# Performance work log

Measured on AMD Instinct MI355X. Metric: run time of the kernel, lower is better.

Reference implementation:

```python
import jax, jax.numpy as jnp
import numpy as np

N, FIN, FOUT = 4096, 256, 256


def setup_inputs() -> dict:
    key = jax.random.key(0)
    ks = jax.random.split(key, 6)
    x = jax.random.normal(ks[0], (N, FIN), jnp.float32)
    adj = jax.random.randint(ks[1], (N, N), 0, 2, jnp.int32)  # dense 0/1 adjacency
    W = jax.random.normal(ks[2], (FOUT, FIN), jnp.float32) / np.sqrt(FIN)
    b = jax.random.normal(ks[3], (FOUT,), jnp.float32) * 0.01
    att_w = jax.random.normal(ks[4], (2 * FOUT,), jnp.float32) / np.sqrt(2.0 * FOUT)  # Linear(2F,1).weight squeezed
    att_b = jax.random.normal(ks[5], (), jnp.float32) * 0.01
    return {"x": x, "adj": adj, "W": W, "b": b, "att_w": att_w, "att_b": att_b}


def reference(x, adj, W, b, att_w, att_b):
    n = x.shape[0]
    fo = W.shape[0]
    h = x @ W.T + b  # [N, Fout]
    # score(i,j) = att([h_i ; h_j]) = h_i.w1 + h_j.w2 + att_b  -> no [N,N,2F] concat
    s = (h @ att_w[:fo])[:, None] + (h @ att_w[fo:])[None, :] + att_b  # [N, N]
    edge = adj == 1
    # GLOBAL softmax over all edges (faithful to F.softmax(stacked_scores, dim=0))
    gmax = jnp.max(jnp.where(edge, s, -jnp.inf))
    e = jnp.exp(s - gmax)
    denom = jnp.sum(jnp.where(edge, e, 0.0))
    p = (e / denom).reshape(-1)  # softmaxed score per pair (valid at edges)
    # original indexes attention_scores[j] by NODE id j into the row-major edge list:
    # recover the score of the j-th global edge (j = 0..N-1) via cumsum rank + scatter
    flat = edge.reshape(-1)
    rank = jnp.cumsum(flat.astype(jnp.int32)) - 1  # rank of each edge in row-major order
    idx = jnp.where(flat, rank, n)  # non-edges and ranks >= n get dropped
    w_node = jnp.zeros((n,), h.dtype).at[idx].set(p, mode="drop")  # [N]
    # output[i] = sum_{j: adj[i,j]==1} w_node[j] * h[j]
    out = jax.nn.relu(edge.astype(h.dtype) @ (w_node[:, None] * h))
    return out
```

## Files before the change

kernel.cpp:

```cpp
#include <hip/hip_runtime.h>
#include <cstdint>
#include <cstddef>

#define NN 4096
#define FDIM 256

typedef __attribute__((ext_vector_type(4))) float fx4;
typedef __attribute__((ext_vector_type(2))) float fx2;
typedef __attribute__((ext_vector_type(8))) short s8v;

__device__ inline uint16_t f2bf(float f) {
    union { float f; uint32_t u; } v; v.f = f;
    uint32_t u = v.u;
    uint32_t r = (u + 0x7FFFu + ((u >> 16) & 1u)) >> 16;
    return (uint16_t)r;
}

__global__ __launch_bounds__(512) void k_h(const float* __restrict__ x,
        const float* __restrict__ W, const float* __restrict__ bias,
        const float* __restrict__ att_w, float* __restrict__ h,
        float* __restrict__ a1p, float* __restrict__ a2p) {
    __shared__ __align__(16) float xs[2][64 * 68];
    __shared__ __align__(16) float wt[2][64 * 68];
    const int bi = blockIdx.x, bf = blockIdx.y;
    const int t = threadIdx.x;
    const int t256 = t & 255;
    const int kh = t >> 8;
    const int tx = t256 & 15, ty = t256 >> 4;
    float acc[4][4] = {};
    float rx[8], rw[8];
    #pragma unroll
    for (int u = 0; u < 8; ++u) {
        const int e = t + 512 * u, r = e >> 6, c = e & 63;
        rx[u] = x[(size_t)(bi * 64 + r) * 256 + c];
        rw[u] = W[(size_t)(bf * 64 + r) * 256 + c];
    }
    for (int p = 0; p < 4; ++p) {
        float* xb = xs[p & 1];
        float* wb = wt[p & 1];
        #pragma unroll
        for (int u = 0; u < 8; ++u) {
            const int e = t + 512 * u, r = e >> 6, c = e & 63;
            const int sw = 8 * ((c & 7) ^ ((c >> 3) & 7));
            xb[c * 68 + (r ^ sw)] = rx[u];
            wb[c * 68 + (r ^ sw)] = rw[u];
        }
        __syncthreads();
        if (p < 3) {
            const int k0 = (p + 1) * 64;
            #pragma unroll
            for (int u = 0; u < 8; ++u) {
                const int e = t + 512 * u, r = e >> 6, c = e & 63;
                rx[u] = x[(size_t)(bi * 64 + r) * 256 + k0 + c];
                rw[u] = W[(size_t)(bf * 64 + r) * 256 + k0 + c];
            }
        }
        #pragma unroll 8
        for (int k = 0; k < 32; ++k) {
            const int kk = kh * 32 + k;
            const int sw = 8 * ((kk & 7) ^ ((kk >> 3) & 7));
            const fx4 av = *(const fx4*)(xb + kk * 68 + ((ty * 4) ^ sw));
            const fx4 bv = *(const fx4*)(wb + kk * 68 + ((tx * 4) ^ sw));
            #pragma unroll
            for (int u = 0; u < 4; ++u)
                #pragma unroll
                for (int v = 0; v < 4; ++v)
                    acc[u][v] += av[u] * bv[v];
        }
    }
    __syncthreads();
    float* cbuf = xs[0];
    if (kh == 1) {
        #pragma unroll
        for (int u = 0; u < 4; ++u)
            *(fx4*)(cbuf + t256 * 16 + u * 4) = *(const fx4*)(&acc[u][0]);
    }
    __syncthreads();
    if (kh == 0) {
        #pragma unroll
        for (int u = 0; u < 4; ++u) {
            const fx4 o = *(const fx4*)(cbuf + t256 * 16 + u * 4);
            #pragma unroll
            for (int v = 0; v < 4; ++v) acc[u][v] += o[v];
        }
        const fx4 bv = *(const fx4*)(bias + bf * 64 + tx * 4);
        const fx4 w1v = *(const fx4*)(att_w + bf * 64 + tx * 4);
        const fx4 w2v = *(const fx4*)(att_w + 256 + bf * 64 + tx * 4);
        #pragma unroll
        for (int u = 0; u < 4; ++u) {
            const int i = bi * 64 + ty * 4 + u;
            fx4 r;
            float s1 = 0.f, s2 = 0.f;
            #pragma unroll
            for (int v = 0; v < 4; ++v) {
                r[v] = acc[u][v] + bv[v];
                s1 += r[v] * w1v[v];
                s2 += r[v] * w2v[v];
            }
            *(fx4*)(h + (size_t)i * 256 + bf * 64 + tx * 4) = r;
            #pragma unroll
            for (int d = 8; d > 0; d >>= 1) {
                s1 += __shfl_down(s1, d, 16);
                s2 += __shfl_down(s2, d, 16);
            }
            if (tx == 0) {
                a1p[bf * NN + i] = s1;
                a2p[bf * NN + i] = s2;
            }
        }
    }
}

__global__ __launch_bounds__(1024) void k_prep(const float* __restrict__ a1p,
        const float* __restrict__ a2p, const int* __restrict__ adj,
        float* __restrict__ E1, float* __restrict__ E2,
        float* __restrict__ wraw, float* __restrict__ Sg) {
    __shared__ float E1s[NN];
    __shared__ float E2s[NN];
    __shared__ float red1[16], red2[16];
    __shared__ int wtot[16];
    __shared__ int base_s;
    const int t = threadIdx.x, lane = t & 63, wv = t >> 6;
    fx4 v1 = {0.f, 0.f, 0.f, 0.f}, v2 = {0.f, 0.f, 0.f, 0.f};
    #pragma unroll
    for (int bf = 0; bf < 4; ++bf) {
        v1 += *(const fx4*)(a1p + bf * NN + t * 4);
        v2 += *(const fx4*)(a2p + bf * NN + t * 4);
    }
    float m1 = fmaxf(fmaxf(v1[0], v1[1]), fmaxf(v1[2], v1[3]));
    float m2 = fmaxf(fmaxf(v2[0], v2[1]), fmaxf(v2[2], v2[3]));
    #pragma unroll
    for (int d = 32; d > 0; d >>= 1) {
        m1 = fmaxf(m1, __shfl_down(m1, d));
        m2 = fmaxf(m2, __shfl_down(m2, d));
    }
    if (lane == 0) { red1[wv] = m1; red2[wv] = m2; }
    __syncthreads();
    if (t == 0) {
        float mm1 = -1e30f, mm2 = -1e30f;
        for (int k = 0; k < 16; ++k) {
            mm1 = fmaxf(mm1, red1[k]);
            mm2 = fmaxf(mm2, red2[k]);
        }
        red1[0] = mm1; red2[0] = mm2;
        *Sg = 0.f;
        base_s = 0;
    }
    __syncthreads();
    const float M1 = red1[0], M2 = red2[0];
    fx4 e1v, e2v, z4 = {0.f, 0.f, 0.f, 0.f};
    #pragma unroll
    for (int j = 0; j < 4; ++j) {
        e1v[j] = expf(v1[j] - M1);
        e2v[j] = expf(v2[j] - M2);
    }
    *(fx4*)(E1s + t * 4) = e1v;
    *(fx4*)(E2s + t * 4) = e2v;
    *(fx4*)(E1 + t * 4) = e1v;
    *(fx4*)(E2 + t * 4) = e2v;
    *(fx4*)(wraw + t * 4) = z4;
    __syncthreads();
    for (int row = 0; row < NN; ++row) {
        const int base = base_s;
        if (base >= NN) break;
        const int4 a = ((const int4*)(adj + (size_t)row * NN))[t];
        const int vj[4] = {a.x, a.y, a.z, a.w};
        int cnt = 0;
        #pragma unroll
        for (int j = 0; j < 4; ++j) cnt += (vj[j] == 1);
        int inc = cnt;
        #pragma unroll
        for (int d = 1; d < 64; d <<= 1) {
            const int y = __shfl_up(inc, d);
            if (lane >= d) inc += y;
        }
        if (lane == 63) wtot[wv] = inc;
        __syncthreads();
        int wbase = 0, total = 0;
        #pragma unroll
        for (int w = 0; w < 16; ++w) {
            const int xw = wtot[w];
            total += xw;
            wbase += (w < wv) ? xw : 0;
        }
        if (t == 0) base_s = base + total;
        int r = base + wbase + inc - cnt;
        if (cnt && r < NN) {
            const float e1 = E1s[row];
            #pragma unroll
            for (int j = 0; j < 4; ++j) {
                if (vj[j] == 1) {
                    if (r < NN) wraw[r] = e1 * E2s[t * 4 + j];
                    ++r;
                }
            }
        }
        __syncthreads();
    }
}

__global__ __launch_bounds__(256) void k_g(const float* __restrict__ h,
        const float* __restrict__ wraw, uint16_t* __restrict__ gt) {
    __shared__ float tile[64 * 33];
    const int bj = blockIdx.x, bf = blockIdx.y;
    const int j0 = bj * 64, f0 = bf * 32;
    const int t = threadIdx.x;
    #pragma unroll
    for (int p = 0; p < 8; ++p) {
        const int e = t + 256 * p;
        const int jl = e >> 5, fl = e & 31;
        tile[jl * 33 + fl] = h[(size_t)(j0 + jl) * 256 + f0 + fl] * wraw[j0 + jl];
    }
    __syncthreads();
    {
        const int fl = t >> 3, cb = t & 7;
        const int phys_cb = cb ^ (fl & 7);
        s8v v;
        #pragma unroll
        for (int lo = 0; lo < 8; ++lo)
            v[lo] = (short)f2bf(tile[(cb * 8 + lo) * 33 + fl]);
        *(s8v*)(gt + (size_t)(f0 + fl) * NN + j0 + phys_cb * 8) = v;
    }
}

__global__ __launch_bounds__(256) void k_fused(const int* __restrict__ adj,
        const uint16_t* __restrict__ gt, const float* __restrict__ E1,
        const float* __restrict__ E2, uint16_t* __restrict__ part,
        float* __restrict__ Sg, int krange) {
    __shared__ __align__(16) uint16_t As[64 * 72];
    __shared__ __align__(16) uint16_t Gs[256 * 64];
    __shared__ __align__(16) uint16_t GsS[16 * 72];
    const int ib = blockIdx.x, ks = blockIdx.y;
    const int t = threadIdx.x;
    const int wv = t >> 6, lane = t & 63;
    const int q = lane >> 4, m16 = lane & 15;
    const int i0 = ib * 64, k0 = ks * krange;
    const int ksteps = krange >> 6;
    fx4 acc[4][4];
    #pragma unroll
    for (int a = 0; a < 4; ++a)
        #pragma unroll
        for (int b = 0; b < 4; ++b) acc[a][b] = (fx4){0.f, 0.f, 0.f, 0.f};
    fx4 accS[4];
    #pragma unroll
    for (int a = 0; a < 4; ++a) accS[a] = (fx4){0.f, 0.f, 0.f, 0.f};
    for (int e = t; e < 15 * 72; e += 256) GsS[72 + e] = 0;

    const int fr = lane >> 3, cb = lane & 7;
    const int ar = t >> 4, ac4 = (t & 15) * 4;
    int4 ra[4];
    #pragma unroll
    for (int p = 0; p < 4; ++p)
        ra[p] = *(const int4*)(adj + (size_t)(i0 + p * 16 + ar) * NN + k0 + ac4);

    for (int step = 0; step < ksteps; ++step) {
        const int kk = k0 + step * 64;
        #pragma unroll
        for (int p = 0; p < 4; ++p) {
            uint2 w;
            w.x = (uint32_t)(ra[p].x | (ra[p].y << 16)) * 0x3F80u;
            w.y = (uint32_t)(ra[p].z | (ra[p].w << 16)) * 0x3F80u;
            *(uint2*)(&As[(p * 16 + ar) * 72 + ac4]) = w;
        }
        #pragma unroll
        for (int p = 0; p < 8; ++p) {
            const int f0 = wv * 64 + p * 8;
            const uint16_t* gp = gt + (size_t)(f0 + fr) * NN + kk + cb * 8;
            __builtin_amdgcn_global_load_lds(
                (const __attribute__((address_space(1))) uint32_t*)gp,
                (__attribute__((address_space(3))) uint32_t*)(Gs + f0 * 64),
                16, 0, 0);
        }
        if (t < 8) {
            const float* e2p = E2 + kk + t * 8;
            uint32_t* dst = (uint32_t*)(&GsS[t * 8]);
            #pragma unroll
            for (int j = 0; j < 4; ++j)
                dst[j] = (uint32_t)f2bf(e2p[2 * j]) |
                         ((uint32_t)f2bf(e2p[2 * j + 1]) << 16);
        }
        __syncthreads();
        if (step + 1 < ksteps) {
            #pragma unroll
            for (int p = 0; p < 4; ++p)
                ra[p] = *(const int4*)(adj + (size_t)(i0 + p * 16 + ar) * NN +
                                       kk + 64 + ac4);
        }
        s8v afr[4][2];
        #pragma unroll
        for (int it = 0; it < 4; ++it)
            #pragma unroll
            for (int kh = 0; kh < 2; ++kh)
                afr[it][kh] = *(const s8v*)(As + (it * 16 + m16) * 72 + kh * 32 + q * 8);
        #pragma unroll
        for (int ft = 0; ft < 4; ++ft) {
            #pragma unroll
            for (int kh = 0; kh < 2; ++kh) {
                const int row = wv * 64 + ft * 16 + m16;
                const int pcb = ((kh << 2) | q) ^ (m16 & 7);
                const s8v bfr = *(const s8v*)(Gs + row * 64 + pcb * 8);
                #pragma unroll
                for (int it = 0; it < 4; ++it)
                    acc[it][ft] = __builtin_amdgcn_mfma_f32_16x16x32_bf16(
                        afr[it][kh], bfr, acc[it][ft], 0, 0, 0);
            }
        }
        if (wv == 3) {
            #pragma unroll
            for (int kh = 0; kh < 2; ++kh) {
                const s8v bfrS = *(const s8v*)(GsS + m16 * 72 + kh * 32 + q * 8);
                #pragma unroll
                for (int it = 0; it < 4; ++it)
                    accS[it] = __builtin_amdgcn_mfma_f32_16x16x32_bf16(
                        afr[it][kh], bfrS, accS[it], 0, 0, 0);
            }
        }
        __syncthreads();
    }
    if (wv == 3) {
        float s_local = 0.f;
        #pragma unroll
        for (int it = 0; it < 4; ++it)
            #pragma unroll
            for (int r = 0; r < 4; ++r)
                s_local += accS[it][r] * E1[i0 + it * 16 + q * 4 + r];
        #pragma unroll
        for (int d = 32; d > 0; d >>= 1) s_local += __shfl_down(s_local, d);
        if (lane == 0) atomicAdd(Sg, s_local);
    }
    uint16_t* dst = part + (size_t)ks * NN * FDIM;
    #pragma unroll
    for (int it = 0; it < 4; ++it) {
        #pragma unroll
        for (int ft = 0; ft < 4; ++ft) {
            const int f = wv * 64 + ft * 16 + m16;
            #pragma unroll
            for (int r = 0; r < 4; ++r) {
                const int i = i0 + it * 16 + q * 4 + r;
                dst[(size_t)i * FDIM + f] = f2bf(acc[it][ft][r]);
            }
        }
    }
}

__global__ __launch_bounds__(256) void k_out(const uint16_t* __restrict__ part,
        const float* __restrict__ Sg, float* __restrict__ out, int nsplit) {
    const size_t idx = ((size_t)blockIdx.x * 256 + threadIdx.x) * 8;
    const float inv = 1.0f / (*Sg);
    float s[8] = {};
    for (int k = 0; k < nsplit; ++k) {
        const s8v v = *(const s8v*)(part + (size_t)k * NN * FDIM + idx);
        #pragma unroll
        for (int j = 0; j < 8; ++j) {
            union { uint32_t u; float f; } cv;
            cv.u = ((uint32_t)(uint16_t)v[j]) << 16;
            s[j] += cv.f;
        }
    }
    fx4 r0, r1;
    #pragma unroll
    for (int j = 0; j < 4; ++j) {
        r0[j] = fmaxf(s[j], 0.f) * inv;
        r1[j] = fmaxf(s[4 + j], 0.f) * inv;
    }
    *(fx4*)(out + idx) = r0;
    *(fx4*)(out + idx + 4) = r1;
}

extern "C" void kernel_launch(void* const* d_in, const int* in_sizes, int n_in,
                              void* d_out, int out_size, void* d_ws, size_t ws_size,
                              hipStream_t stream) {
    const float* x     = (const float*)d_in[0];
    const int*   adj   = (const int*)d_in[1];
    const float* W     = (const float*)d_in[2];
    const float* bias  = (const float*)d_in[3];
    const float* att_w = (const float*)d_in[4];
    float* out = (float*)d_out;
    char* ws = (char*)d_ws;
    float*    h    = (float*)(ws + 0);
    uint16_t* gt   = (uint16_t*)(ws + (size_t)4194304);
    float*    a1p  = (float*)(ws + 6291456);
    float*    a2p  = (float*)(ws + 6356992);
    float*    E1   = (float*)(ws + 6422528);
    float*    E2   = (float*)(ws + 6438912);
    float*    wraw = (float*)(ws + 6455296);
    float*    Sg   = (float*)(ws + 6471680);
    uint16_t* part = (uint16_t*)(ws + 6471936);

    const size_t avail = (ws_size > 6471936) ? (ws_size - 6471936) : 0;
    int splitk = 1;
    while (splitk < 8 &&
           (size_t)(splitk * 2) * NN * FDIM * sizeof(uint16_t) <= avail)
        splitk <<= 1;
    const int krange = NN / splitk;

    k_h    <<<dim3(64, 4), 512, 0, stream>>>(x, W, bias, att_w, h, a1p, a2p);
    k_prep <<<dim3(1), 1024, 0, stream>>>(a1p, a2p, adj, E1, E2, wraw, Sg);
    k_g    <<<dim3(64, 8), 256, 0, stream>>>(h, wraw, gt);
    k_fused<<<dim3(64, splitk), 256, 0, stream>>>(adj, gt, E1, E2, part, Sg, krange);
    k_out  <<<dim3(512), 256, 0, stream>>>(part, Sg, out, splitk);
}
```

Baseline: 146.0 us.

## Fuse all GAT stages into one persistent kernel with grid barriers

Replaces the five separate kernels with a single 256-block persistent kernel that uses atomic-counter grid barriers between phases. The h GEMM now writes the transposed bf16 tile directly, so the separate transpose and scale pass over h is dropped. The aggregation phase uses global_load_lds prefetching and 512-thread blocks with an in-block reduction across wave halves. This removes launch overhead and intermediate traffic, but relies on all blocks being co-resident and serialises the single-block rank scan inside the fused kernel.

After: 287.1 us. 1.97x slower.

```diff
diff --git a/kernel.cpp b/kernel.cpp
--- a/kernel.cpp
+++ b/kernel.cpp
@@ -4,367 +4,413 @@
 
 #define NN 4096
 #define FDIM 256
+#define NBLK 256
 
 typedef __attribute__((ext_vector_type(4))) float fx4;
-typedef __attribute__((ext_vector_type(2))) float fx2;
 typedef __attribute__((ext_vector_type(8))) short s8v;
+
+__device__ int g_cnt;
+__device__ int g_flag;
 
 __device__ inline uint16_t f2bf(float f) {
     union { float f; uint32_t u; } v; v.f = f;
-    uint32_t u = v.u;
-    uint32_t r = (u + 0x7FFFu + ((u >> 16) & 1u)) >> 16;
-    return (uint16_t)r;
+    const uint32_t u = v.u;
+    return (uint16_t)((u + 0x7FFFu + ((u >> 16) & 1u)) >> 16);
 }
 
-__global__ __launch_bounds__(512) void k_h(const float* __restrict__ x,
+struct ShA { float xs[2][64 * 68]; float wt[2][64 * 68]; };
+struct ShP { float E1s[NN]; float E2s[NN]; float red1[8]; float red2[8];
+             int wtot[8]; int base_s; };
+struct ShF { uint16_t As[2][64 * 72]; uint16_t Gs[2][256 * 64]; };
+union ShMem { ShA a; ShP p; ShF f; float cex[4][64 * 68]; };
+
+__device__ __forceinline__ void gbar(int target) {
+    __syncthreads();
+    if (threadIdx.x == 0) {
+        __threadfence();
+        const int prev = __hip_atomic_fetch_add(&g_cnt, 1, __ATOMIC_ACQ_REL,
+                                                __HIP_MEMORY_SCOPE_AGENT);
+        if (prev == target * NBLK - 1) {
+            __hip_atomic_store(&g_flag, target, __ATOMIC_RELEASE,
+                               __HIP_MEMORY_SCOPE_AGENT);
+        } else {
+            while (__hip_atomic_load(&g_flag, __ATOMIC_ACQUIRE,
+                                     __HIP_MEMORY_SCOPE_AGENT) < target)
+                __builtin_amdgcn_s_sleep(2);
+        }
+        __threadfence();
+    }
+    __syncthreads();
+}
+
+__global__ __launch_bounds__(512, 2) void gat_all(
+        const float* __restrict__ x, const int* __restrict__ adj,
         const float* __restrict__ W, const float* __restrict__ bias,
-        const float* __restrict__ att_w, float* __restrict__ h,
-        float* __restrict__ a1p, float* __restrict__ a2p) {
-    __shared__ __align__(16) float xs[2][64 * 68];
-    __shared__ __align__(16) float wt[2][64 * 68];
-    const int bi = blockIdx.x, bf = blockIdx.y;
+        const float* __restrict__ att_w, uint16_t* __restrict__ gt,
+        float* __restrict__ a1p, float* __restrict__ a2p,
+        float* __restrict__ E1, float* __restrict__ E2,
+        float* __restrict__ wraw, float* __restrict__ Sg,
+        uint16_t* __restrict__ part, float* __restrict__ out) {
+    __shared__ __align__(16) ShMem sh;
+    __shared__ int sh_base;
     const int t = threadIdx.x;
-    const int t256 = t & 255;
-    const int kh = t >> 8;
-    const int tx = t256 & 15, ty = t256 >> 4;
-    float acc[4][4] = {};
-    float rx[8], rw[8];
-    #pragma unroll
-    for (int u = 0; u < 8; ++u) {
-        const int e = t + 512 * u, r = e >> 6, c = e & 63;
-        rx[u] = x[(size_t)(bi * 64 + r) * 256 + c];
-        rw[u] = W[(size_t)(bf * 64 + r) * 256 + c];
-    }
-    for (int p = 0; p < 4; ++p) {
-        float* xb = xs[p & 1];
-        float* wb = wt[p & 1];
+    const int b = blockIdx.x;
+    if (t == 0)
+        sh_base = __hip_atomic_load(&g_flag, __ATOMIC_RELAXED, __HIP_MEMORY_SCOPE_AGENT);
+    __syncthreads();
+    const int ep0 = sh_base;
+
+    {
+        const int bi = b & 63, bf = b >> 6;
+        const int t256 = t & 255;
+        const int kh = t >> 8;
+        const int tx = t256 & 15, ty = t256 >> 4;
+        float acc[4][4] = {};
+        float rx[8], rw[8];
         #pragma unroll
         for (int u = 0; u < 8; ++u) {
             const int e = t + 512 * u, r = e >> 6, c = e & 63;
-            const int sw = 8 * ((c & 7) ^ ((c >> 3) & 7));
-            xb[c * 68 + (r ^ sw)] = rx[u];
-            wb[c * 68 + (r ^ sw)] = rw[u];
-        }
-        __syncthreads();
-        if (p < 3) {
-            const int k0 = (p + 1) * 64;
+            rx[u] = x[(size_t)(bi * 64 + r) * 256 + c];
+            rw[u] = W[(size_t)(bf * 64 + r) * 256 + c];
+        }
+        for (int p = 0; p < 4; ++p) {
+            float* xb = sh.a.xs[p & 1];
+            float* wb = sh.a.wt[p & 1];
             #pragma unroll
             for (int u = 0; u < 8; ++u) {
                 const int e = t + 512 * u, r = e >> 6, c = e & 63;
-                rx[u] = x[(size_t)(bi * 64 + r) * 256 + k0 + c];
-                rw[u] = W[(size_t)(bf * 64 + r) * 256 + k0 + c];
-            }
-        }
-        #pragma unroll 8
-        for (int k = 0; k < 32; ++k) {
-            const int kk = kh * 32 + k;
-            const int sw = 8 * ((kk & 7) ^ ((kk >> 3) & 7));
-            const fx4 av = *(const fx4*)(xb + kk * 68 + ((ty * 4) ^ sw));
-            const fx4 bv = *(const fx4*)(wb + kk * 68 + ((tx * 4) ^ sw));
+                const int sw = 8 * ((c & 7) ^ ((c >> 3) & 7));
+                xb[c * 68 + (r ^ sw)] = rx[u];
+                wb[c * 68 + (r ^ sw)] = rw[u];
+            }
+            __syncthreads();
+            if (p < 3) {
+                const int kc = (p + 1) * 64;
+                #pragma unroll
+                for (int u = 0; u < 8; ++u) {
+                    const int e = t + 512 * u, r = e >> 6, c = e & 63;
+                    rx[u] = x[(size_t)(bi * 64 + r) * 256 + kc + c];
+                    rw[u] = W[(size_t)(bf * 64 + r) * 256 + kc + c];
+                }
+            }
+            #pragma unroll 8
+            for (int k = 0; k < 32; ++k) {
+                const int kk = kh * 32 + k;
+                const int sw = 8 * ((kk & 7) ^ ((kk >> 3) & 7));
+                const fx4 av = *(const fx4*)(xb + kk * 68 + ((ty * 4) ^ sw));
+                const fx4 bv = *(const fx4*)(wb + kk * 68 + ((tx * 4) ^ sw));
+                #pragma unroll
+                for (int u = 0; u < 4; ++u)
+                    #pragma unroll
+                    for (int v = 0; v < 4; ++v)
+                        acc[u][v] += av[u] * bv[v];
+            }
+        }
+        __syncthreads();
+        float* cbuf = sh.a.xs[0];
+        if (kh == 1) {
             #pragma unroll
             for (int u = 0; u < 4; ++u)
+                *(fx4*)(cbuf + t256 * 16 + u * 4) = *(const fx4*)(&acc[u][0]);
+        }
+        __syncthreads();
+        if (kh == 0) {
+            float* tileT = sh.a.wt[0];
+            #pragma unroll
+            for (int u = 0; u < 4; ++u) {
+                const fx4 o = *(const fx4*)(cbuf + t256 * 16 + u * 4);
+                #pragma unroll
+                for (int v = 0; v < 4; ++v) acc[u][v] += o[v];
+            }
+            const fx4 bv = *(const fx4*)(bias + bf * 64 + tx * 4);
+            const fx4 w1v = *(const fx4*)(att_w + bf * 64 + tx * 4);
+            const fx4 w2v = *(const fx4*)(att_w + 256 + bf * 64 + tx * 4);
+            #pragma unroll
+            for (int u = 0; u < 4; ++u) {
+                const int i = bi * 64 + ty * 4 + u;
+                fx4 r;
+                float s1 = 0.f, s2 = 0.f;
+                #pragma unroll
+                for (int v = 0; v < 4; ++v) {
+                    r[v] = acc[u][v] + bv[v];
+                    s1 += r[v] * w1v[v];
+                    s2 += r[v] * w2v[v];
+                }
                 #pragma unroll
                 for (int v = 0; v < 4; ++v)
-                    acc[u][v] += av[u] * bv[v];
-        }
-    }
-    __syncthreads();
-    float* cbuf = xs[0];
-    if (kh == 1) {
-        #pragma unroll
-        for (int u = 0; u < 4; ++u)
-            *(fx4*)(cbuf + t256 * 16 + u * 4) = *(const fx4*)(&acc[u][0]);
-    }
-    __syncthreads();
-    if (kh == 0) {
-        #pragma unroll
-        for (int u = 0; u < 4; ++u) {
-            const fx4 o = *(const fx4*)(cbuf + t256 * 16 + u * 4);
-            #pragma unroll
-            for (int v = 0; v < 4; ++v) acc[u][v] += o[v];
-        }
-        const fx4 bv = *(const fx4*)(bias + bf * 64 + tx * 4);
-        const fx4 w1v = *(const fx4*)(att_w + bf * 64 + tx * 4);
-        const fx4 w2v = *(const fx4*)(att_w + 256 + bf * 64 + tx * 4);
-        #pragma unroll
-        for (int u = 0; u < 4; ++u) {
-            const int i = bi * 64 + ty * 4 + u;
-            fx4 r;
-            float s1 = 0.f, s2 = 0.f;
-            #pragma unroll
-            for (int v = 0; v < 4; ++v) {
-                r[v] = acc[u][v] + bv[v];
-                s1 += r[v] * w1v[v];
-                s2 += r[v] * w2v[v];
-            }
-            *(fx4*)(h + (size_t)i * 256 + bf * 64 + tx * 4) = r;
-            #pragma unroll
-            for (int d = 8; d > 0; d >>= 1) {
-                s1 += __shfl_down(s1, d, 16);
-                s2 += __shfl_down(s2, d, 16);
-            }
-            if (tx == 0) {
-                a1p[bf * NN + i] = s1;
-                a2p[bf * NN + i] = s2;
-            }
-        }
-    }
-}
-
-__global__ __launch_bounds__(1024) void k_prep(const float* __restrict__ a1p,
-        const float* __restrict__ a2p, const int* __restrict__ adj,
-        float* __restrict__ E1, float* __restrict__ E2,
-        float* __restrict__ wraw, float* __restrict__ Sg) {
-    __shared__ float E1s[NN];
-    __shared__ float E2s[NN];
-    __shared__ float red1[16], red2[16];
-    __shared__ int wtot[16];
-    __shared__ int base_s;
-    const int t = threadIdx.x, lane = t & 63, wv = t >> 6;
-    fx4 v1 = {0.f, 0.f, 0.f, 0.f}, v2 = {0.f, 0.f, 0.f, 0.f};
+                    tileT[(tx * 4 + v) * 68 + ty * 4 + u] = r[v];
+                #pragma unroll
+                for (int d = 8; d > 0; d >>= 1) {
+                    s1 += __shfl_down(s1, d, 16);
+                    s2 += __shfl_down(s2, d, 16);
+                }
+                if (tx == 0) {
+                    a1p[bf * NN + i] = s1;
+                    a2p[bf * NN + i] = s2;
+                }
+            }
+        }
+        __syncthreads();
+        {
+            const float* tileT = sh.a.wt[0];
+            const int fl = t >> 3, cb = t & 7;
+            const int pcb = cb ^ (fl & 7);
+            s8v v;
+            #pragma unroll
+            for (int lo = 0; lo < 8; ++lo)
+                v[lo] = (short)f2bf(tileT[fl * 68 + cb * 8 + lo]);
+            *(s8v*)(gt + (size_t)(bf * 64 + fl) * NN + bi * 64 + pcb * 8) = v;
+        }
+    }
+
+    gbar(ep0 + 1);
+
+    const int ib = b & 63, ks = b >> 6;
+    const int i0 = ib * 64, k0f = ks * 1024;
+    const int wv = t >> 6, lane = t & 63;
+    const int ar = t >> 4, ac4 = (t & 15) * 4;
+    const int fr = lane >> 3, cbd = lane & 7;
+    int4 ra[2];
     #pragma unroll
-    for (int bf = 0; bf < 4; ++bf) {
-        v1 += *(const fx4*)(a1p + bf * NN + t * 4);
-        v2 += *(const fx4*)(a2p + bf * NN + t * 4);
-    }
-    float m1 = fmaxf(fmaxf(v1[0], v1[1]), fmaxf(v1[2], v1[3]));
-    float m2 = fmaxf(fmaxf(v2[0], v2[1]), fmaxf(v2[2], v2[3]));
+    for (int p = 0; p < 2; ++p)
+        ra[p] = *(const int4*)(adj + (size_t)(i0 + p * 32 + ar) * NN + k0f + ac4);
+
+    if (b == 0) {
+        const int wvi = t >> 6;
+        fx4 v1a = {0.f,0.f,0.f,0.f}, v1b = {0.f,0.f,0.f,0.f};
+        fx4 v2a = {0.f,0.f,0.f,0.f}, v2b = {0.f,0.f,0.f,0.f};
+        #pragma unroll
+        for (int bf = 0; bf < 4; ++bf) {
+            v1a += *(const fx4*)(a1p + bf * NN + t * 8);
+            v1b += *(const fx4*)(a1p + bf * NN + t * 8 + 4);
+            v2a += *(const fx4*)(a2p + bf * NN + t * 8);
+            v2b += *(const fx4*)(a2p + bf * NN + t * 8 + 4);
+        }
+        float m1 = fmaxf(fmaxf(fmaxf(v1a[0], v1a[1]), fmaxf(v1a[2], v1a[3])),
+                         fmaxf(fmaxf(v1b[0], v1b[1]), fmaxf(v1b[2], v1b[3])));
+        float m2 = fmaxf(fmaxf(fmaxf(v2a[0], v2a[1]), fmaxf(v2a[2], v2a[3])),
+                         fmaxf(fmaxf(v2b[0], v2b[1]), fmaxf(v2b[2], v2b[3])));
+        #pragma unroll
+        for (int d = 32; d > 0; d >>= 1) {
+            m1 = fmaxf(m1, __shfl_down(m1, d));
+            m2 = fmaxf(m2, __shfl_down(m2, d));
+        }
+        if (lane == 0) { sh.p.red1[wvi] = m1; sh.p.red2[wvi] = m2; }
+        __syncthreads();
+        if (t == 0) {
+            float mm1 = -1e30f, mm2 = -1e30f;
+            for (int k = 0; k < 8; ++k) {
+                mm1 = fmaxf(mm1, sh.p.red1[k]);
+                mm2 = fmaxf(mm2, sh.p.red2[k]);
+            }
+            sh.p.red1[0] = mm1; sh.p.red2[0] = mm2;
+            *Sg = 0.f;
+            sh.p.base_s = 0;
+        }
+        __syncthreads();
+        const float M1 = sh.p.red1[0], M2 = sh.p.red2[0];
+        fx4 e1a, e1b, e2a, e2b;
+        #pragma unroll
+        for (int j = 0; j < 4; ++j) {
+            e1a[j] = expf(v1a[j] - M1); e1b[j] = expf(v1b[j] - M1);
+            e2a[j] = expf(v2a[j] - M2); e2b[j] = expf(v2b[j] - M2);
+        }
+        *(fx4*)(sh.p.E1s + t * 8) = e1a; *(fx4*)(sh.p.E1s + t * 8 + 4) = e1b;
+        *(fx4*)(sh.p.E2s + t * 8) = e2a; *(fx4*)(sh.p.E2s + t * 8 + 4) = e2b;
+        *(fx4*)(E1 + t * 8) = e1a;       *(fx4*)(E1 + t * 8 + 4) = e1b;
+        *(fx4*)(E2 + t * 8) = e2a;       *(fx4*)(E2 + t * 8 + 4) = e2b;
+        const fx4 z4 = {0.f, 0.f, 0.f, 0.f};
+        *(fx4*)(wraw + t * 8) = z4;      *(fx4*)(wraw + t * 8 + 4) = z4;
+        __syncthreads();
+        for (int row = 0; row < NN; ++row) {
+            const int base = sh.p.base_s;
+            if (base >= NN) break;
+            const int4 a0 = ((const int4*)(adj + (size_t)row * NN))[t * 2];
+            const int4 a1v = ((const int4*)(adj + (size_t)row * NN))[t * 2 + 1];
+            const int vj[8] = {a0.x, a0.y, a0.z, a0.w, a1v.x, a1v.y, a1v.z, a1v.w};
+            int cnt = 0;
+            #pragma unroll
+            for (int j = 0; j < 8; ++j) cnt += (vj[j] == 1);
+            int inc = cnt;
+            #pragma unroll
+            for (int d = 1; d < 64; d <<= 1) {
+                const int y = __shfl_up(inc, d);
+                if (lane >= d) inc += y;
+            }
+            if (lane == 63) sh.p.wtot[wvi] = inc;
+            __syncthreads();
+            int wbase = 0, total = 0;
+            #pragma unroll
+            for (int w = 0; w < 8; ++w) {
+                const int xw = sh.p.wtot[w];
+                total += xw;
+                wbase += (w < wvi) ? xw : 0;
+            }
+            if (t == 0) sh.p.base_s = base + total;
+            int r = base + wbase + inc - cnt;
+            if (cnt && r < NN) {
+                const float e1 = sh.p.E1s[row];
+                #pragma unroll
+                for (int j = 0; j < 8; ++j) {
+                    if (vj[j] == 1) {
+                        if (r < NN) wraw[r] = e1 * sh.p.E2s[t * 8 + j];
+                        ++r;
+                    }
+                }
+            }
+            __syncthreads();
+        }
+    }
+
     #pragma unroll
-    for (int d = 32; d > 0; d >>= 1) {
-        m1 = fmaxf(m1, __shfl_down(m1, d));
-        m2 = fmaxf(m2, __shfl_down(m2, d));
-    }
-    if (lane == 0) { red1[wv] = m1; red2[wv] = m2; }
-    __syncthreads();
-    if (t == 0) {
-        float mm1 = -1e30f, mm2 = -1e30f;
-        for (int k = 0; k < 16; ++k) {
-            mm1 = fmaxf(mm1, red1[k]);
-            mm2 = fmaxf(mm2, red2[k]);
-        }
-        red1[0] = mm1; red2[0] = mm2;
-        *Sg = 0.f;
-        base_s = 0;
-    }
-    __syncthreads();
-    const float M1 = red1[0], M2 = red2[0];
-    fx4 e1v, e2v, z4 = {0.f, 0.f, 0.f, 0.f};
-    #pragma unroll
-    for (int j = 0; j < 4; ++j) {
-        e1v[j] = expf(v1[j] - M1);
-        e2v[j] = expf(v2[j] - M2);
-    }
-    *(fx4*)(E1s + t * 4) = e1v;
-    *(fx4*)(E2s + t * 4) = e2v;
-    *(fx4*)(E1 + t * 4) = e1v;
-    *(fx4*)(E2 + t * 4) = e2v;
-    *(fx4*)(wraw + t * 4) = z4;
-    __syncthreads();
-    for (int row = 0; row < NN; ++row) {
-        const int base = base_s;
-        if (base >= NN) break;
-        const int4 a = ((const int4*)(adj + (size_t)row * NN))[t];
-        const int vj[4] = {a.x, a.y, a.z, a.w};
-        int cnt = 0;
-        #pragma unroll
-        for (int j = 0; j < 4; ++j) cnt += (vj[j] == 1);
-        int inc = cnt;
-        #pragma unroll
-        for (int d = 1; d < 64; d <<= 1) {
-            const int y = __shfl_up(inc, d);
-            if (lane >= d) inc += y;
-        }
-        if (lane == 63) wtot[wv] = inc;
-        __syncthreads();
-        int wbase = 0, total = 0;
-        #pragma unroll
-        for (int w = 0; w < 16; ++w) {
-            const int xw = wtot[w];
-            total += xw;
-            wbase += (w < wv) ? xw : 0;
-        }
-        if (t == 0) base_s = base + total;
-        int r = base + wbase + inc - cnt;
-        if (cnt && r < NN) {
-            const float e1 = E1s[row];
-            #pragma unroll
-            for (int j = 0; j < 4; ++j) {
-                if (vj[j] == 1) {
-                    if (r < NN) wraw[r] = e1 * E2s[t * 4 + j];
-                    ++r;
-                }
-            }
-        }
-        __syncthreads();
-    }
-}
-
-__global__ __launch_bounds__(256) void k_g(const float* __restrict__ h,
-        const float* __restrict__ wraw, uint16_t* __restrict__ gt) {
-    __shared__ float tile[64 * 33];
-    const int bj = blockIdx.x, bf = blockIdx.y;
-    const int j0 = bj * 64, f0 = bf * 32;
-    const int t = threadIdx.x;
-    #pragma unroll
-    for (int p = 0; p < 8; ++p) {
-        const int e = t + 256 * p;
-        const int jl = e >> 5, fl = e & 31;
-        tile[jl * 33 + fl] = h[(size_t)(j0 + jl) * 256 + f0 + fl] * wraw[j0 + jl];
-    }
-    __syncthreads();
+    for (int p = 0; p < 4; ++p) {
+        const uint16_t* gp = gt + (size_t)(wv * 32 + p * 8 + fr) * NN + k0f + cbd * 8;
+        __builtin_amdgcn_global_load_lds(
+            (const __attribute__((address_space(1))) uint32_t*)gp,
+            (__attribute__((address_space(3))) uint32_t*)(&sh.f.Gs[0][(wv * 32 + p * 8) * 64]),
+            16, 0, 0);
+    }
+
+    gbar(ep0 + 2);
+
     {
-        const int fl = t >> 3, cb = t & 7;
-        const int phys_cb = cb ^ (fl & 7);
-        s8v v;
-        #pragma unroll
-        for (int lo = 0; lo < 8; ++lo)
-            v[lo] = (short)f2bf(tile[(cb * 8 + lo) * 33 + fl]);
-        *(s8v*)(gt + (size_t)(f0 + fl) * NN + j0 + phys_cb * 8) = v;
-    }
-}
-
-__global__ __launch_bounds__(256) void k_fused(const int* __restrict__ adj,
-        const uint16_t* __restrict__ gt, const float* __restrict__ E1,
-        const float* __restrict__ E2, uint16_t* __restrict__ part,
-        float* __restrict__ Sg, int krange) {
-    __shared__ __align__(16) uint16_t As[64 * 72];
-    __shared__ __align__(16) uint16_t Gs[256 * 64];
-    __shared__ __align__(16) uint16_t GsS[16 * 72];
-    const int ib = blockIdx.x, ks = blockIdx.y;
-    const int t = threadIdx.x;
-    const int wv = t >> 6, lane = t & 63;
-    const int q = lane >> 4, m16 = lane & 15;
-    const int i0 = ib * 64, k0 = ks * krange;
-    const int ksteps = krange >> 6;
-    fx4 acc[4][4];
-    #pragma unroll
-    for (int a = 0; a < 4; ++a)
-        #pragma unroll
-        for (int b = 0; b < 4; ++b) acc[a][b] = (fx4){0.f, 0.f, 0.f, 0.f};
-    fx4 accS[4];
-    #pragma unroll
-    for (int a = 0; a < 4; ++a) accS[a] = (fx4){0.f, 0.f, 0.f, 0.f};
-    for (int e = t; e < 15 * 72; e += 256) GsS[72 + e] = 0;
-
-    const int fr = lane >> 3, cb = lane & 7;
-    const int ar = t >> 4, ac4 = (t & 15) * 4;
-    int4 ra[4];
-    #pragma unroll
-    for (int p = 0; p < 4; ++p)
-        ra[p] = *(const int4*)(adj + (size_t)(i0 + p * 16 + ar) * NN + k0 + ac4);
-
-    for (int step = 0; step < ksteps; ++step) {
-        const int kk = k0 + step * 64;
-        #pragma unroll
-        for (int p = 0; p < 4; ++p) {
-            uint2 w;
-            w.x = (uint32_t)(ra[p].x | (ra[p].y << 16)) * 0x3F80u;
-            w.y = (uint32_t)(ra[p].z | (ra[p].w << 16)) * 0x3F80u;
-            *(uint2*)(&As[(p * 16 + ar) * 72 + ac4]) = w;
-        }
-        #pragma unroll
-        for (int p = 0; p < 8; ++p) {
-            const int f0 = wv * 64 + p * 8;
-            const uint16_t* gp = gt + (size_t)(f0 + fr) * NN + kk + cb * 8;
-            __builtin_amdgcn_global_load_lds(
-                (const __attribute__((address_space(1))) uint32_t*)gp,
-                (__attribute__((address_space(3))) uint32_t*)(Gs + f0 * 64),
-                16, 0, 0);
-        }
-        if (t < 8) {
-            const float* e2p = E2 + kk + t * 8;
-            uint32_t* dst = (uint32_t*)(&GsS[t * 8]);
-            #pragma unroll
-            for (int j = 0; j < 4; ++j)
-                dst[j] = (uint32_t)f2bf(e2p[2 * j]) |
-                         ((uint32_t)f2bf(e2p[2 * j + 1]) << 16);
-        }
-        __syncthreads();
-        if (step + 1 < ksteps) {
-            #pragma unroll
-            for (int p = 0; p < 4; ++p)
-                ra[p] = *(const int4*)(adj + (size_t)(i0 + p * 16 + ar) * NN +
-                                       kk + 64 + ac4);
-        }
-        s8v afr[4][2];
-        #pragma unroll
-        for (int it = 0; it < 4; ++it)
-            #pragma unroll
-            for (int kh = 0; kh < 2; ++kh)
-                afr[it][kh] = *(const s8v*)(As + (it * 16 + m16) * 72 + kh * 32 + q * 8);
-        #pragma unroll
-        for (int ft = 0; ft < 4; ++ft) {
-            #pragma unroll
-            for (int kh = 0; kh < 2; ++kh) {
-                const int row = wv * 64 + ft * 16 + m16;
-                const int pcb = ((kh << 2) | q) ^ (m16 & 7);
-                const s8v bfr = *(const s8v*)(Gs + row * 64 + pcb * 8);
+        const int q = lane >> 4, m16 = lane & 15;
+        const int khw = wv >> 2, fquad = wv & 3;
+        fx4 acc[4][4];
+        #pragma unroll
+        for (int a2 = 0; a2 < 4; ++a2)
+            #pragma unroll
+            for (int b2 = 0; b2 < 4; ++b2) acc[a2][b2] = (fx4){0.f, 0.f, 0.f, 0.f};
+        float sS = 0.f;
+        const float e1r0 = E1[i0 + ar];
+        const float e1r1 = E1[i0 + 32 + ar];
+        fx4 rw4 = *(const fx4*)(wraw + k0f + ac4);
+        fx4 re2 = *(const fx4*)(E2 + k0f + ac4);
+        {
+            const uint16_t wb0 = f2bf(rw4[0]), wb1 = f2bf(rw4[1]);
+            const uint16_t wb2 = f2bf(rw4[2]), wb3 = f2bf(rw4[3]);
+            #pragma unroll
+            for (int p = 0; p < 2; ++p) {
+                uint2 wo;
+                wo.x = (ra[p].x == 1 ? (uint32_t)wb0 : 0u) |
+                       ((ra[p].y == 1 ? (uint32_t)wb1 : 0u) << 16);
+                wo.y = (ra[p].z == 1 ? (uint32_t)wb2 : 0u) |
+                       ((ra[p].w == 1 ? (uint32_t)wb3 : 0u) << 16);
+                *(uint2*)(&sh.f.As[0][(p * 32 + ar) * 72 + ac4]) = wo;
+            }
+            sS += e1r0 * ((ra[0].x == 1 ? re2[0] : 0.f) + (ra[0].y == 1 ? re2[1] : 0.f) +
+                          (ra[0].z == 1 ? re2[2] : 0.f) + (ra[0].w == 1 ? re2[3] : 0.f));
+            sS += e1r1 * ((ra[1].x == 1 ? re2[0] : 0.f) + (ra[1].y == 1 ? re2[1] : 0.f) +
+                          (ra[1].z == 1 ? re2[2] : 0.f) + (ra[1].w == 1 ? re2[3] : 0.f));
+        }
+        __syncthreads();
+        const int pcb = ((khw << 2) | q) ^ (m16 & 7);
+        for (int stp = 0; stp < 16; ++stp) {
+            const int cur = stp & 1, nxt = cur ^ 1;
+            const int kk = k0f + stp * 64;
+            if (stp < 15) {
+                #pragma unroll
+                for (int p = 0; p < 4; ++p) {
+                    const uint16_t* gp =
+                        gt + (size_t)(wv * 32 + p * 8 + fr) * NN + kk + 64 + cbd * 8;
+                    __builtin_amdgcn_global_load_lds(
+                        (const __attribute__((address_space(1))) uint32_t*)gp,
+                        (__attribute__((address_space(3))) uint32_t*)(&sh.f.Gs[nxt][(wv * 32 + p * 8) * 64]),
+                        16, 0, 0);
+                }
+                #pragma unroll
+                for (int p = 0; p < 2; ++p)
+                    ra[p] = *(const int4*)(adj + (size_t)(i0 + p * 32 + ar) * NN +
+                                           kk + 64 + ac4);
+                rw4 = *(const fx4*)(wraw + kk + 64 + ac4);
+                re2 = *(const fx4*)(E2 + kk + 64 + ac4);
+            }
+            s8v afr[4];
+            #pragma unroll
+            for (int it = 0; it < 4; ++it)
+                afr[it] = *(const s8v*)(&sh.f.As[cur][(it * 16 + m16) * 72 + khw * 32 + q * 8]);
+            #pragma unroll
+            for (int ft = 0; ft < 4; ++ft) {
+                const int row = fquad * 64 + ft * 16 + m16;
+                const s8v bfr = *(const s8v*)(&sh.f.Gs[cur][row * 64 + pcb * 8]);
                 #pragma unroll
                 for (int it = 0; it < 4; ++it)
                     acc[it][ft] = __builtin_amdgcn_mfma_f32_16x16x32_bf16(
-                        afr[it][kh], bfr, acc[it][ft], 0, 0, 0);
-            }
-        }
-        if (wv == 3) {
-            #pragma unroll
-            for (int kh = 0; kh < 2; ++kh) {
-                const s8v bfrS = *(const s8v*)(GsS + m16 * 72 + kh * 32 + q * 8);
-                #pragma unroll
-                for (int it = 0; it < 4; ++it)
-                    accS[it] = __builtin_amdgcn_mfma_f32_16x16x32_bf16(
-                        afr[it][kh], bfrS, accS[it], 0, 0, 0);
-            }
-        }
-        __syncthreads();
-    }
-    if (wv == 3) {
-        float s_local = 0.f;
-        #pragma unroll
-        for (int it = 0; it < 4; ++it)
-            #pragma unroll
-            for (int r = 0; r < 4; ++r)
-                s_local += accS[it][r] * E1[i0 + it * 16 + q * 4 + r];
-        #pragma unroll
-        for (int d = 32; d > 0; d >>= 1) s_local += __shfl_down(s_local, d);
-        if (lane == 0) atomicAdd(Sg, s_local);
-    }
-    uint16_t* dst = part + (size_t)ks * NN * FDIM;
-    #pragma unroll
-    for (int it = 0; it < 4; ++it) {
-        #pragma unroll
-        for (int ft = 0; ft < 4; ++ft) {
-            const int f = wv * 64 + ft * 16 + m16;
-            #pragma unroll
-            for (int r = 0; r < 4; ++r) {
-                const int i = i0 + it * 16 + q * 4 + r;
-                dst[(size_t)i * FDIM + f] = f2bf(acc[it][ft][r]);
-            }
-        }
-    }
-}
-
-__global__ __launch_bounds__(256) void k_out(const uint16_t* __restrict__ part,
-        const float* __restrict__ Sg, float* __restrict__ out, int nsplit) {
-    const size_t idx = ((size_t)blockIdx.x * 256 + threadIdx.x) * 8;
-    const float inv = 1.0f / (*Sg);
-    float s[8] = {};
-    for (int k = 0; k < nsplit; ++k) {
-        const s8v v = *(const s8v*)(part + (size_t)k * NN * FDIM + idx);
-        #pragma unroll
-        for (int j = 0; j < 8; ++j) {
-            union { uint32_t u; float f; } cv;
-            cv.u = ((uint32_t)(uint16_t)v[j]) << 16;
-            s[j] += cv.f;
-        }
-    }
-    fx4 r0, r1;
-    #pragma unroll
-    for (int j = 0; j < 4; ++j) {
-        r0[j] = fmaxf(s[j], 0.f) * inv;
-        r1[j] = fmaxf(s[4 + j], 0.f) * inv;
-    }
-    *(fx4*)(out + idx) = r0;
-    *(fx4*)(out + idx + 4) = r1;
+                        afr[it], bfr, acc[it][ft], 0, 0, 0);
+            }
+            if (stp < 15) {
+                const uint16_t wb0 = f2bf(rw4[0]), wb1 = f2bf(rw4[1]);
+                const uint16_t wb2 = f2bf(rw4[2]), wb3 = f2bf(rw4[3]);
+                #pragma unroll
+                for (int p = 0; p < 2; ++p) {
+                    uint2 wo;
+                    wo.x = (ra[p].x == 1 ? (uint32_t)wb0 : 0u) |
+                           ((ra[p].y == 1 ? (uint32_t)wb1 : 0u) << 16);
+                    wo.y = (ra[p].z == 1 ? (uint32_t)wb2 : 0u) |
+                           ((ra[p].w == 1 ? (uint32_t)wb3 : 0u) << 16);
+                    *(uint2*)(&sh.f.As[nxt][(p * 32 + ar) * 72 + ac4]) = wo;
+                }
+                sS += e1r0 * ((ra[0].x == 1 ? re2[0] : 0.f) + (ra[0].y == 1 ? re2[1] : 0.f) +
+                              (ra[0].z == 1 ? re2[2] : 0.f) + (ra[0].w == 1 ? re2[3] : 0.f));
+                sS += e1r1 * ((ra[1].x == 1 ? re2[0] : 0.f) + (ra[1].y == 1 ? re2[1] : 0.f) +
+                              (ra[1].z == 1 ? re2[2] : 0.f) + (ra[1].w == 1 ? re2[3] : 0.f));
+            }
+            __syncthreads();
+        }
+        #pragma unroll
+        for (int d = 32; d > 0; d >>= 1) sS += __shfl_down(sS, d);
+        if (lane == 0) atomicAdd(Sg, sS);
+        if (wv >= 4) {
+            float* cx = &sh.cex[fquad][0] + lane * 68;
+            #pragma unroll
+            for (int it = 0; it < 4; ++it)
+                #pragma unroll
+                for (int ft = 0; ft < 4; ++ft)
+                    *(fx4*)(cx + it * 16 + ft * 4) = acc[it][ft];
+        }
+        __syncthreads();
+        if (wv < 4) {
+            const float* cx = &sh.cex[fquad][0] + lane * 68;
+            uint16_t* dst = part + (size_t)ks * NN * FDIM;
+            #pragma unroll
+            for (int it = 0; it < 4; ++it)
+                #pragma unroll
+                for (int ft = 0; ft < 4; ++ft) {
+                    const fx4 o = *(const fx4*)(cx + it * 16 + ft * 4);
+                    const int f = fquad * 64 + ft * 16 + m16;
+                    #pragma unroll
+                    for (int r = 0; r < 4; ++r)
+                        dst[(size_t)(i0 + it * 16 + q * 4 + r) * FDIM + f] =
+                            f2bf(acc[it][ft][r] + o[r]);
+                }
+        }
+    }
+
+    gbar(ep0 + 3);
+
+    {
+        const size_t idx = ((size_t)b * 512 + t) * 8;
+        const float inv = 1.0f / (*Sg);
+        float s[8] = {};
+        #pragma unroll
+        for (int k = 0; k < 4; ++k) {
+            const s8v v = *(const s8v*)(part + (size_t)k * NN * FDIM + idx);
+            #pragma unroll
+            for (int j = 0; j < 8; ++j) {
+                union { uint32_t u; float f; } cv;
+                cv.u = ((uint32_t)(uint16_t)v[j]) << 16;
+                s[j] += cv.f;
+            }
+        }
+        fx4 r0, r1;
+        #pragma unroll
+        for (int j = 0; j < 4; ++j) {
+            r0[j] = fmaxf(s[j], 0.f) * inv;
+            r1[j] = fmaxf(s[4 + j], 0.f) * inv;
+        }
+        *(fx4*)(out + idx) = r0;
+        *(fx4*)(out + idx + 4) = r1;
+    }
 }
 
 extern "C" void kernel_launch(void* const* d_in, const int* in_sizes, int n_in,
@@ -377,26 +423,16 @@
     const float* att_w = (const float*)d_in[4];
     float* out = (float*)d_out;
     char* ws = (char*)d_ws;
-    float*    h    = (float*)(ws + 0);
-    uint16_t* gt   = (uint16_t*)(ws + (size_t)4194304);
-    float*    a1p  = (float*)(ws + 6291456);
-    float*    a2p  = (float*)(ws + 6356992);
-    float*    E1   = (float*)(ws + 6422528);
-    float*    E2   = (float*)(ws + 6438912);
-    float*    wraw = (float*)(ws + 6455296);
-    float*    Sg   = (float*)(ws + 6471680);
-    uint16_t* part = (uint16_t*)(ws + 6471936);
-
-    const size_t avail = (ws_size > 6471936) ? (ws_size - 6471936) : 0;
-    int splitk = 1;
-    while (splitk < 8 &&
-           (size_t)(splitk * 2) * NN * FDIM * sizeof(uint16_t) <= avail)
-        splitk <<= 1;
-    const int krange = NN / splitk;
-
-    k_h    <<<dim3(64, 4), 512, 0, stream>>>(x, W, bias, att_w, h, a1p, a2p);
-    k_prep <<<dim3(1), 1024, 0, stream>>>(a1p, a2p, adj, E1, E2, wraw, Sg);
-    k_g    <<<dim3(64, 8), 256, 0, stream>>>(h, wraw, gt);
-    k_fused<<<dim3(64, splitk), 256, 0, stream>>>(adj, gt, E1, E2, part, Sg, krange);
-    k_out  <<<dim3(512), 256, 0, stream>>>(part, Sg, out, splitk);
+    uint16_t* gt   = (uint16_t*)(ws + 0);
+    float*    a1p  = (float*)(ws + 2097152);
+    float*    a2p  = (float*)(ws + 2162688);
+    float*    E1   = (float*)(ws + 2228224);
+    float*    E2   = (float*)(ws + 2244608);
+    float*    wraw = (float*)(ws + 2260992);
+    float*    Sg   = (float*)(ws + 2277376);
+    uint16_t* part = (uint16_t*)(ws + 2277632);
+    (void)in_sizes; (void)n_in; (void)out_size; (void)ws_size;
+
+    gat_all<<<dim3(NBLK), 512, 0, stream>>>(x, adj, W, bias, att_w, gt, a1p, a2p,
+                                            E1, E2, wraw, Sg, part, out);
 }
```
